# Optimization experiments

Measured on AMD Instinct MI355X. Metric: run time of the kernel, lower is better.

Reference implementation:

```python
import jax, jax.numpy as jnp
import numpy as np

E = 8          # num_experts
K = 2          # top_k
TEMP = 1.0     # router_temp
D = 1024       # model dim
H = 4 * D      # expert hidden dim
B, T = 2, 2048


def setup_inputs() -> dict:
    key = jax.random.key(0)
    ks = jax.random.split(key, 5)
    x = jax.random.normal(ks[0], (B, T, D), jnp.float32)
    gate_w = jax.random.normal(ks[1], (D, E), jnp.float32) * 0.02
    gate_b = jnp.zeros((E,), jnp.float32)
    w1 = jax.random.normal(ks[2], (E, D, H), jnp.float32) * 0.02
    b1 = jnp.zeros((E, H), jnp.float32)
    w2 = jax.random.normal(ks[3], (E, H, D), jnp.float32) * 0.02
    b2 = jnp.zeros((E, D), jnp.float32)
    return {"x": x, "gate_w": gate_w, "gate_b": gate_b,
            "w1": w1, "b1": b1, "w2": w2, "b2": b2}


def reference(x, gate_w, gate_b, w1, b1, w2, b2):
    b, t, d = x.shape
    xf = x.reshape(-1, d)                                    # [N, D]
    logits = xf @ gate_w + gate_b                            # [N, E]
    gates = jax.nn.softmax(logits / TEMP, axis=-1)
    topk_gates, topk_idx = jax.lax.top_k(gates, K)           # [N, K]
    topk_gates = topk_gates / (topk_gates.sum(-1, keepdims=True) + 1e-9)
    # combine weight per (token, expert): sum over k slots routed to expert e
    comb = (jax.nn.one_hot(topk_idx, E, dtype=xf.dtype)
            * topk_gates[..., None]).sum(axis=1)             # [N, E]
    out = jnp.zeros_like(xf)
    for e in range(E):  # small fixed loop over experts
        h = jax.nn.gelu(xf @ w1[e] + b1[e], approximate=False)  # exact GELU (torch default)
        out = out + comb[:, e:e + 1] * (h @ w2[e] + b2[e])
    return out.reshape(b, t, d)
```

## Files before the change

### kernel.cpp

```cpp
#include <hip/hip_runtime.h>
#include <math.h>

#define NTOK 4096
#define DIM  1024
#define HID  4096
#define NEXP 8
#define NROW 8192

typedef __bf16 bf16;
typedef __attribute__((ext_vector_type(8))) __bf16 bf16x8;
typedef __attribute__((ext_vector_type(4))) float floatx4;

__device__ __forceinline__ void gl_lds16(const bf16* g, bf16* l) {
    __builtin_amdgcn_global_load_lds(
        (const __attribute__((address_space(1))) void*)g,
        (__attribute__((address_space(3))) void*)l, 16, 0, 0);
}

__global__ void zero_k(int* __restrict__ p) {
    if (threadIdx.x < 16) p[threadIdx.x] = 0;
}

__global__ __launch_bounds__(256) void convx_k(const float* __restrict__ x,
                                               bf16* __restrict__ xb)
{
    size_t gid = (size_t)blockIdx.x * 256 + threadIdx.x;
    size_t eo = gid * 8;
    floatx4 a = *(const floatx4*)(x + eo);
    floatx4 b = *(const floatx4*)(x + eo + 4);
    bf16x8 v;
#pragma unroll
    for (int j = 0; j < 4; ++j) { v[j] = (bf16)a[j]; v[4 + j] = (bf16)b[j]; }
    *(bf16x8*)&xb[eo] = v;
}

__global__ __launch_bounds__(256) void router_k(
    const float* __restrict__ x, const float* __restrict__ gw, const float* __restrict__ gb,
    int* __restrict__ counts, int* __restrict__ tok_e, float* __restrict__ tok_g)
{
    __shared__ __align__(16) float gws[DIM * NEXP];
    int t = threadIdx.x;
#pragma unroll
    for (int i = 0; i < 8; ++i)
        *(floatx4*)&gws[(t * 8 + i) * 4] = *(const floatx4*)&gw[(t * 8 + i) * 4];
    __syncthreads();

    int gid = blockIdx.x * 256 + t;
    int wv = gid >> 6, lane = gid & 63;
    const float* xr = x + (size_t)wv * DIM;
    float acc[NEXP];
#pragma unroll
    for (int e = 0; e < NEXP; ++e) acc[e] = 0.f;
    int d0 = lane * 16;
#pragma unroll
    for (int j = 0; j < 16; ++j) {
        float xv = xr[d0 + j];
#pragma unroll
        for (int e = 0; e < NEXP; ++e) acc[e] += xv * gws[(d0 + j) * NEXP + e];
    }
#pragma unroll
    for (int off = 32; off > 0; off >>= 1) {
#pragma unroll
        for (int e = 0; e < NEXP; ++e) acc[e] += __shfl_xor(acc[e], off, 64);
    }
    if (lane == 0) {
        float lg[NEXP], m = -1e30f;
        for (int e = 0; e < NEXP; ++e) { lg[e] = acc[e] + gb[e]; m = fmaxf(m, lg[e]); }
        float p[NEXP], s = 0.f;
        for (int e = 0; e < NEXP; ++e) { p[e] = expf(lg[e] - m); s += p[e]; }
        int e0 = 0;
        for (int e = 1; e < NEXP; ++e) if (p[e] > p[e0]) e0 = e;
        int e1 = (e0 == 0) ? 1 : 0;
        for (int e = 0; e < NEXP; ++e) if (e != e0 && p[e] > p[e1]) e1 = e;
        float g0 = p[e0] / s, g1 = p[e1] / s;
        float gs = g0 + g1 + 1e-9f;
        g0 /= gs; g1 /= gs;
        tok_e[wv * 2] = e0; tok_e[wv * 2 + 1] = e1;
        tok_g[wv * 2] = g0; tok_g[wv * 2 + 1] = g1;
        atomicAdd(&counts[e0], 1);
        atomicAdd(&counts[e1], 1);
    }
}

__global__ void scan_k(const int* __restrict__ counts, int* __restrict__ base)
{
    if (threadIdx.x == 0) {
        int s = 0;
#pragma unroll
        for (int e = 0; e < NEXP; ++e) { base[e] = s; s += counts[e]; }
        base[NEXP] = s;
    }
}

__global__ __launch_bounds__(256) void scatter_k(
    const int* __restrict__ tok_e, const float* __restrict__ tok_g,
    const int* __restrict__ base, int* __restrict__ counts2,
    int* __restrict__ row_token, float* __restrict__ row_gate, int* __restrict__ tok_row)
{
    int tk = blockIdx.x * 256 + threadIdx.x;
    if (tk >= NTOK) return;
#pragma unroll
    for (int k = 0; k < 2; ++k) {
        int e = tok_e[tk * 2 + k];
        int slot = atomicAdd(&counts2[e], 1);
        int r = base[e] + slot;
        row_token[r] = tk;
        row_gate[r] = tok_g[tk * 2 + k];
        tok_row[tk * 2 + k] = r;
    }
}

__global__ __launch_bounds__(256) void transpose_k(
    const float* __restrict__ src, bf16* __restrict__ dst,
    int R, int sld, size_t soff, size_t es, size_t ed)
{
    int e = blockIdx.z;
    bf16* d = dst + (size_t)e * ed;
    __shared__ __align__(16) bf16 tile[64 * 64];
    int t = threadIdx.x;
    int r0 = blockIdx.y * 64, c0 = blockIdx.x * 64;
#pragma unroll
    for (int i = 0; i < 2; ++i) {
        int c = t + i * 256;
        int rr = c >> 3, cc = c & 7;
        size_t eo = soff + (size_t)e * es + (size_t)(r0 + rr) * sld + c0 + cc * 8;
        floatx4 a = *(const floatx4*)(src + eo);
        floatx4 b = *(const floatx4*)(src + eo + 4);
        bf16x8 v;
#pragma unroll
        for (int j = 0; j < 4; ++j) { v[j] = (bf16)a[j]; v[4 + j] = (bf16)b[j]; }
        *(bf16x8*)&tile[rr * 64 + ((cc ^ ((rr >> 3) & 7)) * 8)] = v;
    }
    __syncthreads();
#pragma unroll
    for (int i = 0; i < 2; ++i) {
        int c = t + i * 256;
        int oc = c >> 3;
        int occ = c & 7;
        bf16x8 v;
#pragma unroll
        for (int j = 0; j < 8; ++j) {
            int r = occ * 8 + j;
            int p = (oc >> 3) ^ ((r >> 3) & 7);
            v[j] = tile[r * 64 + p * 8 + (oc & 7)];
        }
        *(bf16x8*)&d[(size_t)(c0 + oc) * R + r0 + occ * 8] = v;
    }
}

__global__ __launch_bounds__(256) void gemm1_k(
    const bf16* __restrict__ xb, const bf16* __restrict__ w1t, const float* __restrict__ b1,
    const int* __restrict__ counts, const int* __restrict__ base,
    const int* __restrict__ row_token, bf16* __restrict__ hbuf, int Nc, int bias_off)
{
    const int e = blockIdx.z;
    const int cnt = counts[e];
    const int rt = blockIdx.y;
    if (rt * 128 >= cnt) return;
    const int rb = base[e] + rt * 128;
    const int rend = base[e] + cnt;
    const int n0 = blockIdx.x * 128;

    __shared__ __align__(16) bf16 As[3][128 * 32];
    __shared__ __align__(16) bf16 Bs[3][128 * 32];

    const int t = threadIdx.x;
    const int wv = t >> 6, lane = t & 63;
    const int s0 = t, s1 = t + 256;
    const int ar0 = s0 >> 2, ac0 = (s0 & 3) ^ ((s0 >> 3) & 3);
    const int ar1 = s1 >> 2, ac1 = (s1 & 3) ^ ((s1 >> 3) & 3);
    int rr0 = rb + ar0; if (rr0 > NROW - 1) rr0 = NROW - 1;
    int rr1 = rb + ar1; if (rr1 > NROW - 1) rr1 = NROW - 1;
    const bf16* ga0 = xb + (size_t)row_token[rr0] * DIM + ac0 * 8;
    const bf16* ga1 = xb + (size_t)row_token[rr1] * DIM + ac1 * 8;
    const bf16* wb = w1t + (size_t)e * Nc * DIM;
    const bf16* gb0 = wb + (size_t)(n0 + ar0) * DIM + ac0 * 8;
    const bf16* gb1 = wb + (size_t)(n0 + ar1) * DIM + ac1 * 8;
    const int off0 = wv * 512, off1 = 2048 + wv * 512;

    floatx4 acc[4][4];
#pragma unroll
    for (int i = 0; i < 4; ++i)
#pragma unroll
        for (int j = 0; j < 4; ++j) acc[i][j] = floatx4{0.f, 0.f, 0.f, 0.f};

    const int wr = (wv >> 1) * 64, wc = (wv & 1) * 64;
    const int lr = lane & 15;
    const int ck = lane >> 4;

    gl_lds16(ga0,      &As[0][off0]); gl_lds16(ga1,      &As[0][off1]);
    gl_lds16(gb0,      &Bs[0][off0]); gl_lds16(gb1,      &Bs[0][off1]);
    gl_lds16(ga0 + 32, &As[1][off0]); gl_lds16(ga1 + 32, &As[1][off1]);
    gl_lds16(gb0 + 32, &Bs[1][off0]); gl_lds16(gb1 + 32, &Bs[1][off1]);

    const int NSTEP = DIM / 32;
    int bc = 0;
    for (int i = 0; i < NSTEP; ++i) {
        if (i < NSTEP - 1) asm volatile("s_waitcnt vmcnt(4)" ::: "memory");
        else               asm volatile("s_waitcnt vmcnt(0)" ::: "memory");
        __builtin_amdgcn_s_barrier();
        asm volatile("" ::: "memory");
        if (i + 2 < NSTEP) {
            int bs = bc + 2; if (bs >= 3) bs -= 3;
            const int kn = (i + 2) * 32;
            gl_lds16(ga0 + kn, &As[bs][off0]); gl_lds16(ga1 + kn, &As[bs][off1]);
            gl_lds16(gb0 + kn, &Bs[bs][off0]); gl_lds16(gb1 + kn, &Bs[bs][off1]);
        }
        bf16x8 af[4], bg[4];
#pragma unroll
        for (int q = 0; q < 4; ++q) {
            int r = wr + q * 16 + lr;
            af[q] = *(const bf16x8*)&As[bc][r * 32 + ((ck ^ ((r >> 1) & 3)) * 8)];
        }
#pragma unroll
        for (int q = 0; q < 4; ++q) {
            int r = wc + q * 16 + lr;
            bg[q] = *(const bf16x8*)&Bs[bc][r * 32 + ((ck ^ ((r >> 1) & 3)) * 8)];
        }
        __builtin_amdgcn_s_setprio(1);
#pragma unroll
        for (int mi = 0; mi < 4; ++mi)
#pragma unroll
            for (int ni = 0; ni < 4; ++ni)
                acc[mi][ni] = __builtin_amdgcn_mfma_f32_16x16x32_bf16(af[mi], bg[ni], acc[mi][ni], 0, 0, 0);
        __builtin_amdgcn_s_setprio(0);
        bc += 1; if (bc >= 3) bc -= 3;
    }

#pragma unroll
    for (int mi = 0; mi < 4; ++mi) {
#pragma unroll
        for (int r = 0; r < 4; ++r) {
            int m = wr + mi * 16 + (lane >> 4) * 4 + r;
            int gr = rb + m;
            if (gr < rend) {
#pragma unroll
                for (int ni = 0; ni < 4; ++ni) {
                    int col = n0 + wc + ni * 16 + lr;
                    float v = acc[mi][ni][r] + b1[e * HID + bias_off + col];
                    v = 0.5f * v * (1.f + erff(v * 0.70710678f));
                    hbuf[(size_t)gr * Nc + col] = (bf16)v;
                }
            }
        }
    }
}

__global__ __launch_bounds__(256) void gemm2_k(
    const bf16* __restrict__ hbuf, const bf16* __restrict__ w2t, const float* __restrict__ b2,
    const int* __restrict__ counts, const int* __restrict__ base,
    const float* __restrict__ row_gate, float* __restrict__ ybuf,
    int Kc, int first, int last)
{
    const int e = blockIdx.z;
    const int cnt = counts[e];
    const int rt = blockIdx.y;
    if (rt * 128 >= cnt) return;
    const int rb = base[e] + rt * 128;
    const int rend = base[e] + cnt;
    const int n0 = blockIdx.x * 128;

    __shared__ __align__(16) bf16 As[3][128 * 32];
    __shared__ __align__(16) bf16 Bs[3][128 * 32];

    const int t = threadIdx.x;
    const int wv = t >> 6, lane = t & 63;
    const int s0 = t, s1 = t + 256;
    const int ar0 = s0 >> 2, ac0 = (s0 & 3) ^ ((s0 >> 3) & 3);
    const int ar1 = s1 >> 2, ac1 = (s1 & 3) ^ ((s1 >> 3) & 3);
    int rr0 = rb + ar0; if (rr0 > NROW - 1) rr0 = NROW - 1;
    int rr1 = rb + ar1; if (rr1 > NROW - 1) rr1 = NROW - 1;
    const bf16* ga0 = hbuf + (size_t)rr0 * Kc + ac0 * 8;
    const bf16* ga1 = hbuf + (size_t)rr1 * Kc + ac1 * 8;
    const bf16* wb = w2t + (size_t)e * DIM * Kc;
    const bf16* gb0 = wb + (size_t)(n0 + ar0) * Kc + ac0 * 8;
    const bf16* gb1 = wb + (size_t)(n0 + ar1) * Kc + ac1 * 8;
    const int off0 = wv * 512, off1 = 2048 + wv * 512;

    floatx4 acc[4][4];
#pragma unroll
    for (int i = 0; i < 4; ++i)
#pragma unroll
        for (int j = 0; j < 4; ++j) acc[i][j] = floatx4{0.f, 0.f, 0.f, 0.f};

    const int wr = (wv >> 1) * 64, wc = (wv & 1) * 64;
    const int lr = lane & 15;
    const int ck = lane >> 4;

    gl_lds16(ga0,      &As[0][off0]); gl_lds16(ga1,      &As[0][off1]);
    gl_lds16(gb0,      &Bs[0][off0]); gl_lds16(gb1,      &Bs[0][off1]);
    gl_lds16(ga0 + 32, &As[1][off0]); gl_lds16(ga1 + 32, &As[1][off1]);
    gl_lds16(gb0 + 32, &Bs[1][off0]); gl_lds16(gb1 + 32, &Bs[1][off1]);

    const int nstep = Kc >> 5;
    int bc = 0;
    for (int i = 0; i < nstep; ++i) {
        if (i < nstep - 1) asm volatile("s_waitcnt vmcnt(4)" ::: "memory");
        else               asm volatile("s_waitcnt vmcnt(0)" ::: "memory");
        __builtin_amdgcn_s_barrier();
        asm volatile("" ::: "memory");
        if (i + 2 < nstep) {
            int bs = bc + 2; if (bs >= 3) bs -= 3;
            const int kn = (i + 2) * 32;
            gl_lds16(ga0 + kn, &As[bs][off0]); gl_lds16(ga1 + kn, &As[bs][off1]);
            gl_lds16(gb0 + kn, &Bs[bs][off0]); gl_lds16(gb1 + kn, &Bs[bs][off1]);
        }
        bf16x8 af[4], bg[4];
#pragma unroll
        for (int q = 0; q < 4; ++q) {
            int r = wr + q * 16 + lr;
            af[q] = *(const bf16x8*)&As[bc][r * 32 + ((ck ^ ((r >> 1) & 3)) * 8)];
        }
#pragma unroll
        for (int q = 0; q < 4; ++q) {
            int r = wc + q * 16 + lr;
            bg[q] = *(const bf16x8*)&Bs[bc][r * 32 + ((ck ^ ((r >> 1) & 3)) * 8)];
        }
        __builtin_amdgcn_s_setprio(1);
#pragma unroll
        for (int mi = 0; mi < 4; ++mi)
#pragma unroll
            for (int ni = 0; ni < 4; ++ni)
                acc[mi][ni] = __builtin_amdgcn_mfma_f32_16x16x32_bf16(af[mi], bg[ni], acc[mi][ni], 0, 0, 0);
        __builtin_amdgcn_s_setprio(0);
        bc += 1; if (bc >= 3) bc -= 3;
    }

#pragma unroll
    for (int mi = 0; mi < 4; ++mi) {
#pragma unroll
        for (int r = 0; r < 4; ++r) {
            int m = wr + mi * 16 + (lane >> 4) * 4 + r;
            int gr = rb + m;
            if (gr < rend) {
#pragma unroll
                for (int ni = 0; ni < 4; ++ni) {
                    int col = n0 + wc + ni * 16 + lr;
                    size_t idx = (size_t)gr * DIM + col;
                    float v = acc[mi][ni][r];
                    if (last) {
                        float prev = first ? 0.f : ybuf[idx];
                        ybuf[idx] = row_gate[gr] * (prev + v + b2[e * DIM + col]);
                    } else {
                        ybuf[idx] = first ? v : (ybuf[idx] + v);
                    }
                }
            }
        }
    }
}

__global__ __launch_bounds__(256) void combine_k(
    const float* __restrict__ ybuf, const int* __restrict__ tok_row, float* __restrict__ out)
{
    int i = blockIdx.x * 256 + threadIdx.x;
    int tk = i >> 8;
    int dc = (i & 255) * 4;
    int ra = tok_row[tk * 2], rb = tok_row[tk * 2 + 1];
    floatx4 a = *(const floatx4*)&ybuf[(size_t)ra * DIM + dc];
    floatx4 b = *(const floatx4*)&ybuf[(size_t)rb * DIM + dc];
    floatx4 o;
#pragma unroll
    for (int j = 0; j < 4; ++j) o[j] = a[j] + b[j];
    *(floatx4*)&out[(size_t)tk * DIM + dc] = o;
}

extern "C" void kernel_launch(void* const* d_in, const int* in_sizes, int n_in,
                              void* d_out, int out_size, void* d_ws, size_t ws_size,
                              hipStream_t stream)
{
    const float* x  = (const float*)d_in[0];
    const float* gw = (const float*)d_in[1];
    const float* gb = (const float*)d_in[2];
    const float* w1 = (const float*)d_in[3];
    const float* b1 = (const float*)d_in[4];
    const float* w2 = (const float*)d_in[5];
    const float* b2 = (const float*)d_in[6];
    float* out = (float*)d_out;

    char* w = (char*)d_ws;
    int*   counts  = (int*)(w + 0);
    int*   counts2 = (int*)(w + 32);
    int*   base    = (int*)(w + 64);
    int*   tok_e   = (int*)(w + 256);
    float* tok_g   = (float*)(w + 256 + 32768);
    int*   row_tok = (int*)(w + 256 + 2 * 32768);
    float* row_g   = (float*)(w + 256 + 3 * 32768);
    int*   tok_row = (int*)(w + 256 + 4 * 32768);
    size_t off = 256 + 5 * 32768;
    bf16*  xb   = (bf16*)(w + off);   off += (size_t)NTOK * DIM * 2;
    float* ybuf = (float*)(w + off);  off += (size_t)NROW * DIM * 4;

    int Hc = HID;
    for (;;) {
        size_t need = off + (size_t)NEXP * Hc * DIM * 2 + (size_t)NROW * Hc * 2;
        if (need <= ws_size || Hc == 128) break;
        Hc >>= 1;
    }
    bf16* wT   = (bf16*)(w + off);  off += (size_t)NEXP * Hc * DIM * 2;
    bf16* hbuf = (bf16*)(w + off);

    zero_k<<<1, 64, 0, stream>>>(counts);
    router_k<<<NTOK / 4, 256, 0, stream>>>(x, gw, gb, counts, tok_e, tok_g);
    scan_k<<<1, 64, 0, stream>>>(counts, base);
    scatter_k<<<NTOK / 256, 256, 0, stream>>>(tok_e, tok_g, base, counts2, row_tok, row_g, tok_row);
    convx_k<<<(NTOK * DIM) / 2048, 256, 0, stream>>>(x, xb);

    const int nc = HID / Hc;
    for (int ch = 0; ch < nc; ++ch) {
        transpose_k<<<dim3(Hc / 64, DIM / 64, NEXP), 256, 0, stream>>>(
            w1, wT, DIM, HID, (size_t)ch * Hc, (size_t)DIM * HID, (size_t)Hc * DIM);
        gemm1_k<<<dim3(Hc / 128, 32, NEXP), 256, 0, stream>>>(
            xb, wT, b1, counts, base, row_tok, hbuf, Hc, ch * Hc);
        transpose_k<<<dim3(DIM / 64, Hc / 64, NEXP), 256, 0, stream>>>(
            w2, wT, Hc, DIM, (size_t)ch * Hc * DIM, (size_t)HID * DIM, (size_t)DIM * Hc);
        gemm2_k<<<dim3(DIM / 128, 32, NEXP), 256, 0, stream>>>(
            hbuf, wT, b2, counts, base, row_g, ybuf, Hc, ch == 0, ch == nc - 1);
    }

    combine_k<<<NTOK, 256, 0, stream>>>(ybuf, tok_row, out);
}
```

Measured before the change: 741.6 us.

## Split-K gemm2 into two partial buffers and fold gate/bias into combine

gemm2 now splits its K dimension in two across blockIdx.z, with each half writing fp32 partials to a separate ybuf slice. The gate scaling and b2 bias move into combine_k, which sums both partials per routed row. Both GEMMs also drop from a triple-buffered, two-ahead LDS prefetch to double buffering with a full vmcnt(0) wait each step. The aim is more blocks for gemm2, which has only N=1024, to fill the CUs, at the cost of an extra 32MB partial buffer write/read and less load latency hiding in the GEMM main loops.

```diff
diff --git a/kernel.cpp b/kernel.cpp
--- a/kernel.cpp
+++ b/kernel.cpp
@@ -6,6 +6,7 @@
 #define HID  4096
 #define NEXP 8
 #define NROW 8192
+#define KSPLIT 2
 
 typedef __bf16 bf16;
 typedef __attribute__((ext_vector_type(8))) __bf16 bf16x8;
@@ -161,8 +162,8 @@
     const int rend = base[e] + cnt;
     const int n0 = blockIdx.x * 128;
 
-    __shared__ __align__(16) bf16 As[3][128 * 32];
-    __shared__ __align__(16) bf16 Bs[3][128 * 32];
+    __shared__ __align__(16) bf16 As[2][128 * 32];
+    __shared__ __align__(16) bf16 Bs[2][128 * 32];
 
     const int t = threadIdx.x;
     const int wv = t >> 6, lane = t & 63;
@@ -188,23 +189,19 @@
     const int lr = lane & 15;
     const int ck = lane >> 4;
 
-    gl_lds16(ga0,      &As[0][off0]); gl_lds16(ga1,      &As[0][off1]);
-    gl_lds16(gb0,      &Bs[0][off0]); gl_lds16(gb1,      &Bs[0][off1]);
-    gl_lds16(ga0 + 32, &As[1][off0]); gl_lds16(ga1 + 32, &As[1][off1]);
-    gl_lds16(gb0 + 32, &Bs[1][off0]); gl_lds16(gb1 + 32, &Bs[1][off1]);
+    gl_lds16(ga0, &As[0][off0]); gl_lds16(ga1, &As[0][off1]);
+    gl_lds16(gb0, &Bs[0][off0]); gl_lds16(gb1, &Bs[0][off1]);
 
     const int NSTEP = DIM / 32;
-    int bc = 0;
     for (int i = 0; i < NSTEP; ++i) {
-        if (i < NSTEP - 1) asm volatile("s_waitcnt vmcnt(4)" ::: "memory");
-        else               asm volatile("s_waitcnt vmcnt(0)" ::: "memory");
+        const int bc = i & 1;
+        asm volatile("s_waitcnt vmcnt(0)" ::: "memory");
         __builtin_amdgcn_s_barrier();
         asm volatile("" ::: "memory");
-        if (i + 2 < NSTEP) {
-            int bs = bc + 2; if (bs >= 3) bs -= 3;
-            const int kn = (i + 2) * 32;
-            gl_lds16(ga0 + kn, &As[bs][off0]); gl_lds16(ga1 + kn, &As[bs][off1]);
-            gl_lds16(gb0 + kn, &Bs[bs][off0]); gl_lds16(gb1 + kn, &Bs[bs][off1]);
+        if (i + 1 < NSTEP) {
+            const int kn = (i + 1) * 32;
+            gl_lds16(ga0 + kn, &As[bc ^ 1][off0]); gl_lds16(ga1 + kn, &As[bc ^ 1][off1]);
+            gl_lds16(gb0 + kn, &Bs[bc ^ 1][off0]); gl_lds16(gb1 + kn, &Bs[bc ^ 1][off1]);
         }
         bf16x8 af[4], bg[4];
 #pragma unroll
@@ -224,7 +221,6 @@
             for (int ni = 0; ni < 4; ++ni)
                 acc[mi][ni] = __builtin_amdgcn_mfma_f32_16x16x32_bf16(af[mi], bg[ni], acc[mi][ni], 0, 0, 0);
         __builtin_amdgcn_s_setprio(0);
-        bc += 1; if (bc >= 3) bc -= 3;
     }
 
 #pragma unroll
@@ -247,21 +243,23 @@
 }
 
 __global__ __launch_bounds__(256) void gemm2_k(
-    const bf16* __restrict__ hbuf, const bf16* __restrict__ w2t, const float* __restrict__ b2,
+    const bf16* __restrict__ hbuf, const bf16* __restrict__ w2t,
     const int* __restrict__ counts, const int* __restrict__ base,
-    const float* __restrict__ row_gate, float* __restrict__ ybuf,
-    int Kc, int first, int last)
-{
-    const int e = blockIdx.z;
+    float* __restrict__ ybuf, int Kc, int first)
+{
+    const int e  = blockIdx.z >> 1;
+    const int ks = blockIdx.z & 1;
     const int cnt = counts[e];
     const int rt = blockIdx.y;
     if (rt * 128 >= cnt) return;
     const int rb = base[e] + rt * 128;
     const int rend = base[e] + cnt;
     const int n0 = blockIdx.x * 128;
-
-    __shared__ __align__(16) bf16 As[3][128 * 32];
-    __shared__ __align__(16) bf16 Bs[3][128 * 32];
+    const int klen = Kc / KSPLIT;
+    const int kbeg = ks * klen;
+
+    __shared__ __align__(16) bf16 As[2][128 * 32];
+    __shared__ __align__(16) bf16 Bs[2][128 * 32];
 
     const int t = threadIdx.x;
     const int wv = t >> 6, lane = t & 63;
@@ -270,11 +268,11 @@
     const int ar1 = s1 >> 2, ac1 = (s1 & 3) ^ ((s1 >> 3) & 3);
     int rr0 = rb + ar0; if (rr0 > NROW - 1) rr0 = NROW - 1;
     int rr1 = rb + ar1; if (rr1 > NROW - 1) rr1 = NROW - 1;
-    const bf16* ga0 = hbuf + (size_t)rr0 * Kc + ac0 * 8;
-    const bf16* ga1 = hbuf + (size_t)rr1 * Kc + ac1 * 8;
+    const bf16* ga0 = hbuf + (size_t)rr0 * Kc + kbeg + ac0 * 8;
+    const bf16* ga1 = hbuf + (size_t)rr1 * Kc + kbeg + ac1 * 8;
     const bf16* wb = w2t + (size_t)e * DIM * Kc;
-    const bf16* gb0 = wb + (size_t)(n0 + ar0) * Kc + ac0 * 8;
-    const bf16* gb1 = wb + (size_t)(n0 + ar1) * Kc + ac1 * 8;
+    const bf16* gb0 = wb + (size_t)(n0 + ar0) * Kc + kbeg + ac0 * 8;
+    const bf16* gb1 = wb + (size_t)(n0 + ar1) * Kc + kbeg + ac1 * 8;
     const int off0 = wv * 512, off1 = 2048 + wv * 512;
 
     floatx4 acc[4][4];
@@ -287,23 +285,19 @@
     const int lr = lane & 15;
     const int ck = lane >> 4;
 
-    gl_lds16(ga0,      &As[0][off0]); gl_lds16(ga1,      &As[0][off1]);
-    gl_lds16(gb0,      &Bs[0][off0]); gl_lds16(gb1,      &Bs[0][off1]);
-    gl_lds16(ga0 + 32, &As[1][off0]); gl_lds16(ga1 + 32, &As[1][off1]);
-    gl_lds16(gb0 + 32, &Bs[1][off0]); gl_lds16(gb1 + 32, &Bs[1][off1]);
-
-    const int nstep = Kc >> 5;
-    int bc = 0;
+    gl_lds16(ga0, &As[0][off0]); gl_lds16(ga1, &As[0][off1]);
+    gl_lds16(gb0, &Bs[0][off0]); gl_lds16(gb1, &Bs[0][off1]);
+
+    const int nstep = klen >> 5;
     for (int i = 0; i < nstep; ++i) {
-        if (i < nstep - 1) asm volatile("s_waitcnt vmcnt(4)" ::: "memory");
-        else               asm volatile("s_waitcnt vmcnt(0)" ::: "memory");
+        const int bc = i & 1;
+        asm volatile("s_waitcnt vmcnt(0)" ::: "memory");
         __builtin_amdgcn_s_barrier();
         asm volatile("" ::: "memory");
-        if (i + 2 < nstep) {
-            int bs = bc + 2; if (bs >= 3) bs -= 3;
-            const int kn = (i + 2) * 32;
-            gl_lds16(ga0 + kn, &As[bs][off0]); gl_lds16(ga1 + kn, &As[bs][off1]);
-            gl_lds16(gb0 + kn, &Bs[bs][off0]); gl_lds16(gb1 + kn, &Bs[bs][off1]);
+        if (i + 1 < nstep) {
+            const int kn = (i + 1) * 32;
+            gl_lds16(ga0 + kn, &As[bc ^ 1][off0]); gl_lds16(ga1 + kn, &As[bc ^ 1][off1]);
+            gl_lds16(gb0 + kn, &Bs[bc ^ 1][off0]); gl_lds16(gb1 + kn, &Bs[bc ^ 1][off1]);
         }
         bf16x8 af[4], bg[4];
 #pragma unroll
@@ -323,9 +317,9 @@
             for (int ni = 0; ni < 4; ++ni)
                 acc[mi][ni] = __builtin_amdgcn_mfma_f32_16x16x32_bf16(af[mi], bg[ni], acc[mi][ni], 0, 0, 0);
         __builtin_amdgcn_s_setprio(0);
-        bc += 1; if (bc >= 3) bc -= 3;
-    }
-
+    }
+
+    float* yb = ybuf + (size_t)ks * NROW * DIM;
 #pragma unroll
     for (int mi = 0; mi < 4; ++mi) {
 #pragma unroll
@@ -338,12 +332,7 @@
                     int col = n0 + wc + ni * 16 + lr;
                     size_t idx = (size_t)gr * DIM + col;
                     float v = acc[mi][ni][r];
-                    if (last) {
-                        float prev = first ? 0.f : ybuf[idx];
-                        ybuf[idx] = row_gate[gr] * (prev + v + b2[e * DIM + col]);
-                    } else {
-                        ybuf[idx] = first ? v : (ybuf[idx] + v);
-                    }
+                    yb[idx] = first ? v : (yb[idx] + v);
                 }
             }
         }
@@ -351,17 +340,28 @@
 }
 
 __global__ __launch_bounds__(256) void combine_k(
-    const float* __restrict__ ybuf, const int* __restrict__ tok_row, float* __restrict__ out)
+    const float* __restrict__ ybuf, const int* __restrict__ tok_row,
+    const int* __restrict__ tok_e, const float* __restrict__ tok_g,
+    const float* __restrict__ b2, float* __restrict__ out)
 {
     int i = blockIdx.x * 256 + threadIdx.x;
     int tk = i >> 8;
     int dc = (i & 255) * 4;
-    int ra = tok_row[tk * 2], rb = tok_row[tk * 2 + 1];
-    floatx4 a = *(const floatx4*)&ybuf[(size_t)ra * DIM + dc];
-    floatx4 b = *(const floatx4*)&ybuf[(size_t)rb * DIM + dc];
+    int ra = tok_row[tk * 2], rbx = tok_row[tk * 2 + 1];
+    int ea = tok_e[tk * 2],  eb = tok_e[tk * 2 + 1];
+    float ga = tok_g[tk * 2], gbv = tok_g[tk * 2 + 1];
+    const float* y0 = ybuf;
+    const float* y1 = ybuf + (size_t)NROW * DIM;
+    floatx4 a0 = *(const floatx4*)&y0[(size_t)ra * DIM + dc];
+    floatx4 a1 = *(const floatx4*)&y1[(size_t)ra * DIM + dc];
+    floatx4 b0 = *(const floatx4*)&y0[(size_t)rbx * DIM + dc];
+    floatx4 b1v = *(const floatx4*)&y1[(size_t)rbx * DIM + dc];
+    floatx4 b2a = *(const floatx4*)&b2[ea * DIM + dc];
+    floatx4 b2b = *(const floatx4*)&b2[eb * DIM + dc];
     floatx4 o;
 #pragma unroll
-    for (int j = 0; j < 4; ++j) o[j] = a[j] + b[j];
+    for (int j = 0; j < 4; ++j)
+        o[j] = ga * (a0[j] + a1[j] + b2a[j]) + gbv * (b0[j] + b1v[j] + b2b[j]);
     *(floatx4*)&out[(size_t)tk * DIM + dc] = o;
 }
 
@@ -389,7 +389,7 @@
     int*   tok_row = (int*)(w + 256 + 4 * 32768);
     size_t off = 256 + 5 * 32768;
     bf16*  xb   = (bf16*)(w + off);   off += (size_t)NTOK * DIM * 2;
-    float* ybuf = (float*)(w + off);  off += (size_t)NROW * DIM * 4;
+    float* ybuf = (float*)(w + off);  off += (size_t)KSPLIT * NROW * DIM * 4;
 
     int Hc = HID;
     for (;;) {
@@ -414,9 +414,9 @@
             xb, wT, b1, counts, base, row_tok, hbuf, Hc, ch * Hc);
         transpose_k<<<dim3(DIM / 64, Hc / 64, NEXP), 256, 0, stream>>>(
             w2, wT, Hc, DIM, (size_t)ch * Hc * DIM, (size_t)HID * DIM, (size_t)DIM * Hc);
-        gemm2_k<<<dim3(DIM / 128, 32, NEXP), 256, 0, stream>>>(
-            hbuf, wT, b2, counts, base, row_g, ybuf, Hc, ch == 0, ch == nc - 1);
-    }
-
-    combine_k<<<NTOK, 256, 0, stream>>>(ybuf, tok_row, out);
-}
+        gemm2_k<<<dim3(DIM / 128, 32, NEXP * KSPLIT), 256, 0, stream>>>(
+            hbuf, wT, counts, base, ybuf, Hc, ch == 0);
+    }
+
+    combine_k<<<NTOK, 256, 0, stream>>>(ybuf, tok_row, tok_e, tok_g, b2, out);
+}
```

New measurement: 723.1 us. 2.5% less time.
